# Kernel tuning notes

Hardware: AMD Instinct MI355X
Metric: run time of the kernel (lower is better)

Reference implementation:

```python
import jax, jax.numpy as jnp
import numpy as np

EPS = 1e-5

def mish(x):
    return x * jnp.tanh(jnp.logaddexp(x, 0.0))

def instance_norm(x, gamma, beta):
    # x: (N, C, D, H, W); normalize per (N, C) over spatial dims
    mu = jnp.mean(x, axis=(2, 3, 4), keepdims=True)
    var = jnp.var(x, axis=(2, 3, 4), keepdims=True)
    xh = (x - mu) * jax.lax.rsqrt(var + EPS)
    return xh * gamma[None, :, None, None, None] + beta[None, :, None, None, None]

def conv3d(x, w, stride, padding):
    return jax.lax.conv_general_dilated(
        x, w, window_strides=(stride, stride, stride), padding=padding,
        dimension_numbers=('NCDHW', 'OIDHW', 'NCDHW'))

def pad_k(k, p):
    # center-pad kernel spatial dims up to 5x5x5
    return jnp.pad(k, ((0, 0), (0, 0), (p, p), (p, p), (p, p)))

def mode_conv(x, t, c5, c3, c1, a3, a5, gw, gb, gamma, beta):
    N = x.shape[0]
    Co = c5.shape[0]
    # gate: Linear(num_tasks -> 5*Co), softmax over the 5 experts
    g = jax.nn.softmax((t @ gw.T + gb).reshape(N, 5, Co), axis=1)  # (N,5,Co)
    pool3 = jnp.full((3, 3, 3), 1.0 / 27.0, x.dtype)
    pool5 = jnp.full((5, 5, 5), 1.0 / 125.0, x.dtype)
    experts = jnp.stack([
        c5,                      # conv5x5
        pad_k(c3, 1),            # conv3x3 padded to 5
        pad_k(c1, 2),            # conv1x1 padded to 5
        pad_k(a3 * pool3, 1),    # avg3x3: (Co,Ci,1,1,1)*(3,3,3) broadcast, padded
        a5 * pool5,              # avg5x5
    ], axis=0)                   # (5, Co, Ci, 5, 5, 5)
    # per-sample synthesized kernel
    w = jnp.einsum('eoidhw,neo->noidhw', experts, g)  # (N, Co, Ci, 5,5,5)
    # per-sample conv3d, padding 'same' (training branch of original)
    y = jax.vmap(lambda xi, wi: conv3d(xi[None], wi, 1, 'SAME')[0])(x, w)
    return mish(instance_norm(y, gamma, beta))

def setup_inputs() -> dict:
    key = jax.random.key(0)
    ks = jax.random.split(key, 32)
    N, Ci, Co, T = 2, 32, 64, 10
    D = H = W = 64
    f32 = jnp.float32
    def kconv(k, co, ci, ksz, fan):
        bound = float(np.sqrt(6.0 / ((1.0 + 5.0) * fan)))  # kaiming_uniform a=sqrt(5), fan_out
        return jax.random.uniform(k, (co, ci, ksz, ksz, ksz), f32, -bound, bound)
    inp = {}
    inp['x'] = jax.random.normal(ks[0], (N, Ci, D, H, W), f32)
    inp['t'] = jax.random.normal(ks[1], (N, T), f32)
    def layer(base, ci, co):
        p = {}
        p['conv5'] = kconv(ks[base + 0], co, ci, 5, co * 125)
        p['conv3'] = kconv(ks[base + 1], co, ci, 3, co * 27)
        p['conv1'] = kconv(ks[base + 2], co, ci, 1, co)
        p['avg3'] = kconv(ks[base + 3], co, ci, 1, co)
        p['avg5'] = kconv(ks[base + 4], co, ci, 1, co)
        gb_bound = 1.0 / np.sqrt(T)
        p['gw'] = jax.random.uniform(ks[base + 5], (5 * co, T), f32, -gb_bound, gb_bound)
        p['gb'] = jax.random.uniform(ks[base + 6], (5 * co,), f32, -gb_bound, gb_bound)
        p['gamma'] = jnp.ones((co,), f32)
        p['beta'] = jnp.zeros((co,), f32)
        return p
    for name, v in layer(2, Ci, Co).items():
        inp['l1_' + name] = v
    for name, v in layer(12, Co, Co).items():
        inp['l2_' + name] = v
    dw_bound = float(np.sqrt(1.0 / (Co * 8)))
    inp['down_w'] = jax.random.uniform(ks[25], (Co, Co, 2, 2, 2), f32, -dw_bound, dw_bound)
    inp['down_gamma'] = jnp.ones((Co,), f32)
    inp['down_beta'] = jnp.zeros((Co,), f32)
    return inp

def reference(x, t,
              l1_conv5, l1_conv3, l1_conv1, l1_avg3, l1_avg5, l1_gw, l1_gb, l1_gamma, l1_beta,
              l2_conv5, l2_conv3, l2_conv1, l2_avg3, l2_avg5, l2_gw, l2_gb, l2_gamma, l2_beta,
              down_w, down_gamma, down_beta):
    h = mode_conv(x, t, l1_conv5, l1_conv3, l1_conv1, l1_avg3, l1_avg5, l1_gw, l1_gb, l1_gamma, l1_beta)
    x_skip = mode_conv(h, t, l2_conv5, l2_conv3, l2_conv1, l2_avg3, l2_avg5, l2_gw, l2_gb, l2_gamma, l2_beta)
    y = conv3d(x_skip, down_w, 2, 'VALID')
    y = mish(instance_norm(y, down_gamma, down_beta))
    return (y, x_skip)
```

## Files before the change

kernel.cpp:

```cpp
#include <hip/hip_runtime.h>
#include <cstdint>
#include <cstddef>

constexpr int NB  = 2;
constexpr int CO  = 64;
constexpr int DIM = 64;
constexpr int SP  = DIM * DIM * DIM;
constexpr int NC  = NB * CO;
constexpr int Y_SZ = NB * CO * 32 * 32 * 32;

typedef float f32x4 __attribute__((ext_vector_type(4)));
typedef short s16x8 __attribute__((ext_vector_type(8)));

__device__ __forceinline__ unsigned short f2bf(float f) {
    unsigned int u = __float_as_uint(f);
    unsigned int r = (u + 0x7fffu + ((u >> 16) & 1u)) >> 16;
    return (unsigned short)r;
}
__device__ __forceinline__ float bf2f(unsigned short u) {
    return __uint_as_float((unsigned int)u << 16);
}
__device__ __forceinline__ unsigned int pack2(float a, float b) {
    return (unsigned int)f2bf(a) | ((unsigned int)f2bf(b) << 16);
}
__device__ __forceinline__ float mish_f(float x) {
    float e = __expf(x);
    float num = e * (e + 2.f);
    float r = x * num * __builtin_amdgcn_rcpf(num + 2.f);
    return (x > 15.f) ? x : r;
}

__device__ __forceinline__ void gload_lds16(const void* g, void* l) {
    __builtin_amdgcn_global_load_lds(
        (const __attribute__((address_space(1))) unsigned int*)g,
        (__attribute__((address_space(3))) unsigned int*)l, 16, 0, 0);
}

__global__ void gate_kernel(const float* __restrict__ t, const float* __restrict__ gw,
                            const float* __restrict__ gb, float* __restrict__ g,
                            float* __restrict__ zbuf) {
    int tid = threadIdx.x;
    if (tid >= 128) { if (tid < 192) zbuf[tid - 128] = 0.f; return; }
    int n = tid >> 6, co = tid & 63;
    float tl[10];
#pragma unroll
    for (int k = 0; k < 10; ++k) tl[k] = t[n * 10 + k];
    float l[5];
#pragma unroll
    for (int e = 0; e < 5; ++e) {
        int row = e * CO + co;
        float acc = gb[row];
#pragma unroll
        for (int k = 0; k < 10; ++k) acc += tl[k] * gw[row * 10 + k];
        l[e] = acc;
    }
    float m = l[0];
#pragma unroll
    for (int e = 1; e < 5; ++e) m = fmaxf(m, l[e]);
    float s = 0.f;
#pragma unroll
    for (int e = 0; e < 5; ++e) { l[e] = expf(l[e] - m); s += l[e]; }
    float inv = 1.f / s;
#pragma unroll
    for (int e = 0; e < 5; ++e) g[(n * 5 + e) * CO + co] = l[e] * inv;
}

template <int CI>
__global__ void synth_kernel(const float* __restrict__ g,
                             const float* __restrict__ c5, const float* __restrict__ c3,
                             const float* __restrict__ c1, const float* __restrict__ a3,
                             const float* __restrict__ a5, unsigned short* __restrict__ wbuf) {
    int idx = blockIdx.x * 256 + threadIdx.x;
    constexpr int TOTAL = NB * CO * CI * 125;
    if (idx >= TOTAL) return;
    int tap = idx % 125;
    int ci  = (idx / 125) % CI;
    int co  = (idx / (125 * CI)) % CO;
    int n   = idx / (125 * CI * CO);
    const float* gn = g + n * 5 * CO;
    float g0 = gn[0 * CO + co], g1 = gn[1 * CO + co], g2 = gn[2 * CO + co],
          g3 = gn[3 * CO + co], g4 = gn[4 * CO + co];
    int dz = tap / 25, dy = (tap / 5) % 5, dx = tap % 5;
    int oc = co * CI + ci;
    float v = g0 * c5[(size_t)oc * 125 + tap] + g4 * a5[oc] * (1.f / 125.f);
    if (dz >= 1 && dz <= 3 && dy >= 1 && dy <= 3 && dx >= 1 && dx <= 3)
        v += g1 * c3[(size_t)oc * 27 + (dz - 1) * 9 + (dy - 1) * 3 + (dx - 1)]
           + g3 * a3[oc] * (1.f / 27.f);
    if (dz == 2 && dy == 2 && dx == 2) v += g2 * c1[oc];
    int t = (dy * 5 + dx);
    int cich = ci >> 5, cil = ci & 31;
    wbuf[((((size_t)(n * 5 + dz) * (CI / 32) + cich) * 25 + t) * 64 + co) * 32 + cil] = f2bf(v);
}

__global__ __launch_bounds__(256) void x_to_cl(const float* __restrict__ x,
                                               unsigned short* __restrict__ xcl) {
    __shared__ float ld[32][256];
    int b = blockIdx.x;
    int n = b >> 10;
    size_t base = (size_t)(b & 1023) * 256;
    int tid = threadIdx.x;
    const float* xp = x + (size_t)n * 32 * SP + base + tid;
#pragma unroll
    for (int c = 0; c < 32; ++c) ld[c][tid] = xp[(size_t)c * SP];
    __syncthreads();
    uint4* op = (uint4*)(xcl + ((size_t)n * SP + base) * 32);
#pragma unroll
    for (int r = 0; r < 4; ++r) {
        int idx = r * 256 + tid;
        int px = idx >> 2, q = idx & 3;
        uint4 o;
        o.x = pack2(ld[q * 8 + 0][px], ld[q * 8 + 1][px]);
        o.y = pack2(ld[q * 8 + 2][px], ld[q * 8 + 3][px]);
        o.z = pack2(ld[q * 8 + 4][px], ld[q * 8 + 5][px]);
        o.w = pack2(ld[q * 8 + 6][px], ld[q * 8 + 7][px]);
        op[idx] = o;
    }
}

template <int CI, bool OUT_CL, int PCH>
__global__ __launch_bounds__(512, 4) void conv5_mfma(const unsigned short* __restrict__ xin,
                                                     const unsigned short* __restrict__ wbuf,
                                                     void* __restrict__ outp,
                                                     float* __restrict__ part,
                                                     const void* __restrict__ zbuf) {
    constexpr int NCH = CI / 32;
    constexpr int NS  = 5 * NCH;
    __shared__ __align__(16) unsigned short lds[2][12800];

    const int b   = blockIdx.x;
    const int xt  = b & 3;
    const int yt  = (b >> 2) & 3;
    const int z   = (b >> 4) & 63;
    const int n   = b >> 10;
    const int tid = threadIdx.x;
    const int lane = tid & 63, wv = tid >> 6;
    const int xl = lane & 15, kh = lane >> 4;
    const int yh = wv >> 2, cq = wv & 3;

    f32x4 acc[8];
#pragma unroll
    for (int pt = 0; pt < 8; ++pt)
#pragma unroll
        for (int j = 0; j < 4; ++j) acc[pt][j] = 0.f;

    long goff[4]; int gval[4];
#pragma unroll
    for (int r = 0; r < 4; ++r) {
        int idx = tid + r * 512;
        int p = idx >> 2, khs = idx & 3;
        int xx = p % 20, yy = p / 20;
        int yi = yt * 16 - 2 + yy, xi = xt * 16 - 2 + xx;
        gval[r] = ((unsigned)yi < 64u) && ((unsigned)xi < 64u);
        goff[r] = ((long)(yi * 64 + xi) * CI + khs * 8) * 2;
    }

    auto stage = [&](int s, int buf) {
        int dz = s / NCH, cich = s % NCH;
        int zi = z + dz - 2;
        bool zok = (unsigned)zi < 64u;
        const char* pb = (const char*)xin
                       + ((size_t)(n * SP + zi * 4096) * CI + cich * 32) * 2;
        char* lb = (char*)&lds[buf][0];
#pragma unroll
        for (int r = 0; r < 4; ++r) {
            int idx = tid + r * 512;
            if (idx < 1600) {
                const void* g = (zok && gval[r]) ? (const void*)(pb + goff[r]) : zbuf;
                gload_lds16(g, lb + idx * 16);
            }
        }
    };

    auto compute = [&](int s, int buf) {
        int dz = s / NCH, cich = s % NCH;
        const unsigned short* wp = wbuf
            + ((size_t)((n * 5 + dz) * NCH + cich) * 25) * 2048
            + cq * 512 + xl * 32 + kh * 8;
        const char* src = (const char*)&lds[buf][0];
        __builtin_amdgcn_s_setprio(1);
#pragma unroll 1
        for (int dx = 0; dx < 5; ++dx) {
            int xx = xl + dx;
            s16x8 fr[12];
#pragma unroll
            for (int r = 0; r < 12; ++r) {
                int row = yh * 8 + r;
                fr[r] = *(const s16x8*)(src + (size_t)(row * 20 + xx) * 64 + kh * 16);
            }
#pragma unroll
            for (int dy = 0; dy < 5; ++dy) {
                s16x8 a = *(const s16x8*)(wp + (size_t)(dy * 5 + dx) * 2048);
#pragma unroll
                for (int pt = 0; pt < 8; ++pt)
                    acc[pt] = __builtin_amdgcn_mfma_f32_16x16x32_bf16(
                        a, fr[pt + dy], acc[pt], 0, 0, 0);
            }
        }
        __builtin_amdgcn_s_setprio(0);
    };

    stage(0, 0);
    __syncthreads();
#pragma unroll 1
    for (int s = 0; s < NS; ++s) {
        if (s + 1 < NS) stage(s + 1, (s + 1) & 1);
        compute(s, s & 1);
        __syncthreads();
    }

    {
        float s1[4], s2[4];
#pragma unroll
        for (int j = 0; j < 4; ++j) { s1[j] = 0.f; s2[j] = 0.f; }
#pragma unroll
        for (int pt = 0; pt < 8; ++pt)
#pragma unroll
            for (int j = 0; j < 4; ++j) {
                float v = acc[pt][j];
                s1[j] += v; s2[j] += v * v;
            }
#pragma unroll
        for (int o = 1; o < 16; o <<= 1)
#pragma unroll
            for (int j = 0; j < 4; ++j) {
                s1[j] += __shfl_xor(s1[j], o, 64);
                s2[j] += __shfl_xor(s2[j], o, 64);
            }
        if (xl == 0) {
            int co = cq * 16 + kh * 4;
            int cb = (b & 1023) * 2 + yh;
#pragma unroll
            for (int j = 0; j < 4; ++j) {
                part[((size_t)(n * 2 + 0) * 64 + co + j) * PCH + cb] = s1[j];
                part[((size_t)(n * 2 + 1) * 64 + co + j) * PCH + cb] = s2[j];
            }
        }
    }

    if (OUT_CL) {
        char* tb = (char*)&lds[0][0];
#pragma unroll
        for (int pt = 0; pt < 8; ++pt) {
            int pix = (yh * 8 + pt) * 16 + xl;
            unsigned int ad = ((unsigned)(pix * 128 + cq * 32 + kh * 8))
                              ^ ((unsigned)(pix & 7) << 4);
            *(unsigned int*)(tb + ad)     = pack2(acc[pt][0], acc[pt][1]);
            *(unsigned int*)(tb + ad + 4) = pack2(acc[pt][2], acc[pt][3]);
        }
        __syncthreads();
#pragma unroll
        for (int it = 0; it < 4; ++it) {
            int idx = it * 512 + tid;
            int pix = idx >> 3, ch = idx & 7;
            uint4 v = *(const uint4*)(tb + (((unsigned)idx * 16)
                                            ^ ((unsigned)(pix & 7) << 4)));
            int y = yt * 16 + (pix >> 4), x = xt * 16 + (pix & 15);
            *(uint4*)((unsigned short*)outp
                      + ((size_t)(n * SP + z * 4096 + y * 64 + x) * 64 + ch * 8)) = v;
        }
    } else {
        float* op = (float*)outp;
#pragma unroll
        for (int pt = 0; pt < 8; ++pt) {
            int y = yt * 16 + yh * 8 + pt;
#pragma unroll
            for (int j = 0; j < 4; ++j)
                op[((size_t)(n * 64 + cq * 16 + kh * 4 + j) * 64 + z) * 4096
                   + y * 64 + xt * 16 + xl] = acc[pt][j];
        }
    }
}

template <int CH>
__global__ void stats_fin(const float* __restrict__ part, float* __restrict__ st,
                          float invS) {
    int blk = blockIdx.x;
    int n = blk >> 6, co = blk & 63;
    int tid = threadIdx.x;
    const float* ps = part + ((size_t)(n * 2 + 0) * 64 + co) * CH;
    const float* pq = part + ((size_t)(n * 2 + 1) * 64 + co) * CH;
    float s1 = 0.f, s2 = 0.f;
    for (int i = tid; i < CH; i += 256) { s1 += ps[i]; s2 += pq[i]; }
#pragma unroll
    for (int o = 1; o < 64; o <<= 1) {
        s1 += __shfl_xor(s1, o, 64);
        s2 += __shfl_xor(s2, o, 64);
    }
    __shared__ float sh1[4], sh2[4];
    if ((tid & 63) == 0) { sh1[tid >> 6] = s1; sh2[tid >> 6] = s2; }
    __syncthreads();
    if (tid == 0) {
        float a = sh1[0] + sh1[1] + sh1[2] + sh1[3];
        float q = sh2[0] + sh2[1] + sh2[2] + sh2[3];
        float mean = a * invS;
        float var  = q * invS - mean * mean;
        st[(n * 64 + co) * 2]     = mean;
        st[(n * 64 + co) * 2 + 1] = rsqrtf(var + 1e-5f);
    }
}

__global__ void norm_mish_cl_kernel(unsigned short* __restrict__ h,
                                    const float* __restrict__ st,
                                    const float* __restrict__ gamma,
                                    const float* __restrict__ beta) {
    size_t idx = (size_t)blockIdx.x * 256 + threadIdx.x;
    uint4 v = ((uint4*)h)[idx];
    int c0 = ((int)(idx & 7)) * 8;
    size_t pix = idx >> 3;
    int n = (int)(pix >> 18);
    unsigned int* pv = &v.x;
#pragma unroll
    for (int q = 0; q < 4; ++q) {
        unsigned int wv = pv[q];
        unsigned int out = 0;
#pragma unroll
        for (int hv = 0; hv < 2; ++hv) {
            int c = c0 + 2 * q + hv;
            int nc = n * 64 + c;
            float val = bf2f((unsigned short)((wv >> (16 * hv)) & 0xffffu));
            float xh = (val - st[nc * 2]) * st[nc * 2 + 1] * gamma[c] + beta[c];
            out |= ((unsigned int)f2bf(mish_f(xh))) << (16 * hv);
        }
        pv[q] = out;
    }
    ((uint4*)h)[idx] = v;
}

template <int SHIFT>
__global__ void norm_mish_kernel(float* __restrict__ buf, const float* __restrict__ stats,
                                 const float* __restrict__ gamma, const float* __restrict__ beta,
                                 int total4) {
    int idx = blockIdx.x * 256 + threadIdx.x;
    if (idx >= total4) return;
    float4 v = reinterpret_cast<float4*>(buf)[idx];
    int nc = idx >> (SHIFT - 2);
    int c  = nc & 63;
    float mean = stats[nc * 2], inv = stats[nc * 2 + 1];
    float ga = gamma[c], be = beta[c];
    float* pv = &v.x;
#pragma unroll
    for (int k = 0; k < 4; ++k) {
        float xh = (pv[k] - mean) * inv * ga + be;
        pv[k] = mish_f(xh);
    }
    reinterpret_cast<float4*>(buf)[idx] = v;
}

__global__ __launch_bounds__(256) void down_conv_kernel(float* __restrict__ xin,
                                                        const float* __restrict__ dw,
                                                        const float* __restrict__ st,
                                                        const float* __restrict__ gamma,
                                                        const float* __restrict__ beta,
                                                        float* __restrict__ out,
                                                        float* __restrict__ part) {
    __shared__ float ls[8][2][8][64];
    int b   = blockIdx.x;
    int yt  = b & 7;
    int z   = (b >> 3) & 31;
    int n   = b >> 8;
    int tid = threadIdx.x;
    int xo  = tid & 31;
    int cog = tid >> 5;

    float acc[4][8];
#pragma unroll
    for (int yo = 0; yo < 4; ++yo)
#pragma unroll
        for (int j = 0; j < 8; ++j) acc[yo][j] = 0.f;

    for (int cc = 0; cc < 8; ++cc) {
        for (int idx = tid; idx < 8192; idx += 256) {
            int xx = idx & 63;
            int yy = (idx >> 6) & 7;
            int dz = (idx >> 9) & 1;
            int c  = idx >> 10;
            int ci = cc * 8 + c;
            size_t ga = ((size_t)(n * CO + ci) * 64 + 2 * z + dz) * 4096
                      + (yt * 8 + yy) * 64 + xx;
            float v = xin[ga];
            int nc = n * 64 + ci;
            float nv = mish_f((v - st[nc * 2]) * st[nc * 2 + 1] * gamma[ci] + beta[ci]);
            ls[c][dz][yy][xx] = nv;
            xin[ga] = nv;
        }
        __syncthreads();
#pragma unroll 1
        for (int c = 0; c < 8; ++c) {
            int ci = cc * 8 + c;
#pragma unroll
            for (int tap = 0; tap < 8; ++tap) {
                int dz = tap >> 2, dy = (tap >> 1) & 1, dx = tap & 1;
                float w[8];
#pragma unroll
                for (int j = 0; j < 8; ++j)
                    w[j] = dw[((size_t)(cog * 8 + j) * CO + ci) * 8 + tap];
#pragma unroll
                for (int yo = 0; yo < 4; ++yo) {
                    float xv = ls[c][dz][yo * 2 + dy][2 * xo + dx];
#pragma unroll
                    for (int j = 0; j < 8; ++j) acc[yo][j] += w[j] * xv;
                }
            }
        }
        __syncthreads();
    }
#pragma unroll
    for (int yo = 0; yo < 4; ++yo)
#pragma unroll
        for (int j = 0; j < 8; ++j)
            out[((size_t)(n * CO + cog * 8 + j) * 32 + z) * 1024 + (yt * 4 + yo) * 32 + xo]
                = acc[yo][j];

    float s1[8], s2[8];
#pragma unroll
    for (int j = 0; j < 8; ++j) { s1[j] = 0.f; s2[j] = 0.f; }
#pragma unroll
    for (int yo = 0; yo < 4; ++yo)
#pragma unroll
        for (int j = 0; j < 8; ++j) {
            float v = acc[yo][j];
            s1[j] += v; s2[j] += v * v;
        }
#pragma unroll
    for (int o = 1; o < 32; o <<= 1)
#pragma unroll
        for (int j = 0; j < 8; ++j) {
            s1[j] += __shfl_xor(s1[j], o, 64);
            s2[j] += __shfl_xor(s2[j], o, 64);
        }
    if (xo == 0) {
        int cb = b & 255;
#pragma unroll
        for (int j = 0; j < 8; ++j) {
            int co = cog * 8 + j;
            part[((size_t)(n * 2 + 0) * 64 + co) * 256 + cb] = s1[j];
            part[((size_t)(n * 2 + 1) * 64 + co) * 256 + cb] = s2[j];
        }
    }
}

extern "C" void kernel_launch(void* const* d_in, const int* in_sizes, int n_in,
                              void* d_out, int out_size, void* d_ws, size_t ws_size,
                              hipStream_t stream) {
    const float* x      = (const float*)d_in[0];
    const float* t      = (const float*)d_in[1];
    const float* l1_c5  = (const float*)d_in[2];
    const float* l1_c3  = (const float*)d_in[3];
    const float* l1_c1  = (const float*)d_in[4];
    const float* l1_a3  = (const float*)d_in[5];
    const float* l1_a5  = (const float*)d_in[6];
    const float* l1_gw  = (const float*)d_in[7];
    const float* l1_gb  = (const float*)d_in[8];
    const float* l1_ga  = (const float*)d_in[9];
    const float* l1_be  = (const float*)d_in[10];
    const float* l2_c5  = (const float*)d_in[11];
    const float* l2_c3  = (const float*)d_in[12];
    const float* l2_c1  = (const float*)d_in[13];
    const float* l2_a3  = (const float*)d_in[14];
    const float* l2_a5  = (const float*)d_in[15];
    const float* l2_gw  = (const float*)d_in[16];
    const float* l2_gb  = (const float*)d_in[17];
    const float* l2_ga  = (const float*)d_in[18];
    const float* l2_be  = (const float*)d_in[19];
    const float* down_w = (const float*)d_in[20];
    const float* dn_ga  = (const float*)d_in[21];
    const float* dn_be  = (const float*)d_in[22];

    char* ws = (char*)d_ws;
    unsigned short* xcl = (unsigned short*)(ws);
    unsigned short* h2  = (unsigned short*)(ws + 33554432);
    unsigned short* w1  = (unsigned short*)(ws + 100663296);
    unsigned short* w2  = (unsigned short*)(ws + 101687296);
    float* g1    = (float*)(ws + 103735296);
    float* g2    = (float*)(ws + 103737856);
    float* st1   = (float*)(ws + 103740416);
    float* st2   = (float*)(ws + 103741440);
    float* st3   = (float*)(ws + 103742464);
    float* part1 = (float*)(ws + 103743488);
    float* part2 = (float*)(ws + 105840640);
    float* part3 = (float*)(ws + 107937792);
    float* zbuf  = (float*)(ws + 108199936);

    float* yout  = (float*)d_out;
    float* xskip = (float*)d_out + Y_SZ;

    gate_kernel<<<1, 192, 0, stream>>>(t, l1_gw, l1_gb, g1, zbuf);
    gate_kernel<<<1, 192, 0, stream>>>(t, l2_gw, l2_gb, g2, zbuf);
    synth_kernel<32><<<(NB * CO * 32 * 125 + 255) / 256, 256, 0, stream>>>(
        g1, l1_c5, l1_c3, l1_c1, l1_a3, l1_a5, w1);
    synth_kernel<64><<<(NB * CO * 64 * 125 + 255) / 256, 256, 0, stream>>>(
        g2, l2_c5, l2_c3, l2_c1, l2_a3, l2_a5, w2);
    x_to_cl<<<2048, 256, 0, stream>>>(x, xcl);

    conv5_mfma<32, true, 2048><<<2048, 512, 0, stream>>>(xcl, w1, h2, part1, zbuf);
    stats_fin<2048><<<128, 256, 0, stream>>>(part1, st1, 1.f / SP);
    norm_mish_cl_kernel<<<16384, 256, 0, stream>>>(h2, st1, l1_ga, l1_be);

    conv5_mfma<64, false, 2048><<<2048, 512, 0, stream>>>(h2, w2, xskip, part2, zbuf);
    stats_fin<2048><<<128, 256, 0, stream>>>(part2, st2, 1.f / SP);

    down_conv_kernel<<<NB * 32 * 8, 256, 0, stream>>>(xskip, down_w, st2, l2_ga, l2_be,
                                                      yout, part3);
    stats_fin<256><<<128, 256, 0, stream>>>(part3, st3, 1.f / 32768.f);
    norm_mish_kernel<15><<<(NC * 32768 / 4 + 255) / 256, 256, 0, stream>>>(
        yout, st3, dn_ga, dn_be, NC * 32768 / 4);
}
```

Before: 851.5 us.

## Store second conv output as bf16 channels-last and fuse launch stages

The second conv now writes its output as a bf16 channels-last buffer instead of fp32 NCDHW. The down-conv kernel reads that buffer with vector loads, applies norm+mish, and writes the fp32 x_skip. The gate and synth kernels are merged into single launches, and the conv block index is remapped by a stride-8 swizzle. This cuts conv2 write traffic and the down-conv read-modify-write, but the down-conv's scattered fp32 stores to x_skip may be poorly coalesced. Rounding the conv2 output to bf16 before normalization also adds precision loss.

```diff
diff --git a/kernel.cpp b/kernel.cpp
--- a/kernel.cpp
+++ b/kernel.cpp
@@ -36,12 +36,20 @@
         (__attribute__((address_space(3))) unsigned int*)l, 16, 0, 0);
 }
 
-__global__ void gate_kernel(const float* __restrict__ t, const float* __restrict__ gw,
-                            const float* __restrict__ gb, float* __restrict__ g,
-                            float* __restrict__ zbuf) {
+__global__ void gate2_kernel(const float* __restrict__ t,
+                             const float* __restrict__ gw1, const float* __restrict__ gb1,
+                             float* __restrict__ g1,
+                             const float* __restrict__ gw2, const float* __restrict__ gb2,
+                             float* __restrict__ g2,
+                             float* __restrict__ zbuf) {
     int tid = threadIdx.x;
-    if (tid >= 128) { if (tid < 192) zbuf[tid - 128] = 0.f; return; }
-    int n = tid >> 6, co = tid & 63;
+    if (tid < 64) zbuf[tid] = 0.f;
+    int layer = tid >> 7;
+    int lt = tid & 127;
+    int n = lt >> 6, co = lt & 63;
+    const float* gw = layer ? gw2 : gw1;
+    const float* gb = layer ? gb2 : gb1;
+    float* g = layer ? g2 : g1;
     float tl[10];
 #pragma unroll
     for (int k = 0; k < 10; ++k) tl[k] = t[n * 10 + k];
@@ -66,13 +74,11 @@
 }
 
 template <int CI>
-__global__ void synth_kernel(const float* __restrict__ g,
-                             const float* __restrict__ c5, const float* __restrict__ c3,
-                             const float* __restrict__ c1, const float* __restrict__ a3,
-                             const float* __restrict__ a5, unsigned short* __restrict__ wbuf) {
-    int idx = blockIdx.x * 256 + threadIdx.x;
-    constexpr int TOTAL = NB * CO * CI * 125;
-    if (idx >= TOTAL) return;
+__device__ __forceinline__ void synth_one(int idx, const float* __restrict__ g,
+                                          const float* __restrict__ c5, const float* __restrict__ c3,
+                                          const float* __restrict__ c1, const float* __restrict__ a3,
+                                          const float* __restrict__ a5,
+                                          unsigned short* __restrict__ wbuf) {
     int tap = idx % 125;
     int ci  = (idx / 125) % CI;
     int co  = (idx / (125 * CI)) % CO;
@@ -92,6 +98,23 @@
     wbuf[((((size_t)(n * 5 + dz) * (CI / 32) + cich) * 25 + t) * 64 + co) * 32 + cil] = f2bf(v);
 }
 
+__global__ void synth2_kernel(const float* __restrict__ g1,
+                              const float* __restrict__ c51, const float* __restrict__ c31,
+                              const float* __restrict__ c11, const float* __restrict__ a31,
+                              const float* __restrict__ a51, unsigned short* __restrict__ w1,
+                              const float* __restrict__ g2,
+                              const float* __restrict__ c52, const float* __restrict__ c32,
+                              const float* __restrict__ c12, const float* __restrict__ a32,
+                              const float* __restrict__ a52, unsigned short* __restrict__ w2) {
+    constexpr int T1 = NB * CO * 32 * 125;
+    constexpr int T2 = NB * CO * 64 * 125;
+    int idx = blockIdx.x * 256 + threadIdx.x;
+    if (idx < T1)
+        synth_one<32>(idx, g1, c51, c31, c11, a31, a51, w1);
+    else if (idx < T1 + T2)
+        synth_one<64>(idx - T1, g2, c52, c32, c12, a32, a52, w2);
+}
+
 __global__ __launch_bounds__(256) void x_to_cl(const float* __restrict__ x,
                                                unsigned short* __restrict__ xcl) {
     __shared__ float ld[32][256];
@@ -117,17 +140,18 @@
     }
 }
 
-template <int CI, bool OUT_CL, int PCH>
+template <int CI, int PCH>
 __global__ __launch_bounds__(512, 4) void conv5_mfma(const unsigned short* __restrict__ xin,
                                                      const unsigned short* __restrict__ wbuf,
-                                                     void* __restrict__ outp,
+                                                     unsigned short* __restrict__ outp,
                                                      float* __restrict__ part,
                                                      const void* __restrict__ zbuf) {
     constexpr int NCH = CI / 32;
     constexpr int NS  = 5 * NCH;
     __shared__ __align__(16) unsigned short lds[2][12800];
 
-    const int b   = blockIdx.x;
+    const int bid = blockIdx.x;
+    const int b   = (bid & 7) * 256 + (bid >> 3);
     const int xt  = b & 3;
     const int yt  = (b >> 2) & 3;
     const int z   = (b >> 4) & 63;
@@ -237,7 +261,7 @@
         }
     }
 
-    if (OUT_CL) {
+    {
         char* tb = (char*)&lds[0][0];
 #pragma unroll
         for (int pt = 0; pt < 8; ++pt) {
@@ -255,18 +279,8 @@
             uint4 v = *(const uint4*)(tb + (((unsigned)idx * 16)
                                             ^ ((unsigned)(pix & 7) << 4)));
             int y = yt * 16 + (pix >> 4), x = xt * 16 + (pix & 15);
-            *(uint4*)((unsigned short*)outp
+            *(uint4*)(outp
                       + ((size_t)(n * SP + z * 4096 + y * 64 + x) * 64 + ch * 8)) = v;
-        }
-    } else {
-        float* op = (float*)outp;
-#pragma unroll
-        for (int pt = 0; pt < 8; ++pt) {
-            int y = yt * 16 + yh * 8 + pt;
-#pragma unroll
-            for (int j = 0; j < 4; ++j)
-                op[((size_t)(n * 64 + cq * 16 + kh * 4 + j) * 64 + z) * 4096
-                   + y * 64 + xt * 16 + xl] = acc[pt][j];
         }
     }
 }
@@ -346,11 +360,12 @@
     reinterpret_cast<float4*>(buf)[idx] = v;
 }
 
-__global__ __launch_bounds__(256) void down_conv_kernel(float* __restrict__ xin,
+__global__ __launch_bounds__(256) void down_conv_kernel(const unsigned short* __restrict__ h3,
                                                         const float* __restrict__ dw,
                                                         const float* __restrict__ st,
                                                         const float* __restrict__ gamma,
                                                         const float* __restrict__ beta,
+                                                        float* __restrict__ xskip,
                                                         float* __restrict__ out,
                                                         float* __restrict__ part) {
     __shared__ float ls[8][2][8][64];
@@ -369,19 +384,28 @@
         for (int j = 0; j < 8; ++j) acc[yo][j] = 0.f;
 
     for (int cc = 0; cc < 8; ++cc) {
-        for (int idx = tid; idx < 8192; idx += 256) {
-            int xx = idx & 63;
-            int yy = (idx >> 6) & 7;
-            int dz = (idx >> 9) & 1;
-            int c  = idx >> 10;
-            int ci = cc * 8 + c;
-            size_t ga = ((size_t)(n * CO + ci) * 64 + 2 * z + dz) * 4096
-                      + (yt * 8 + yy) * 64 + xx;
-            float v = xin[ga];
-            int nc = n * 64 + ci;
-            float nv = mish_f((v - st[nc * 2]) * st[nc * 2 + 1] * gamma[ci] + beta[ci]);
-            ls[c][dz][yy][xx] = nv;
-            xin[ga] = nv;
+#pragma unroll
+        for (int r = 0; r < 4; ++r) {
+            int p  = r * 256 + tid;
+            int xx = p & 63, yy = (p >> 6) & 7, dz = p >> 9;
+            int zi = 2 * z + dz, yi = yt * 8 + yy;
+            size_t pix = (size_t)n * SP + (size_t)zi * 4096 + yi * 64 + xx;
+            uint4 v = *(const uint4*)(h3 + pix * 64 + cc * 8);
+            unsigned int* pv = &v.x;
+#pragma unroll
+            for (int q = 0; q < 4; ++q) {
+#pragma unroll
+                for (int hv = 0; hv < 2; ++hv) {
+                    int c  = 2 * q + hv;
+                    int ci = cc * 8 + c;
+                    int nc = n * 64 + ci;
+                    float val = bf2f((unsigned short)((pv[q] >> (16 * hv)) & 0xffffu));
+                    float nv  = mish_f((val - st[nc * 2]) * st[nc * 2 + 1] * gamma[ci]
+                                       + beta[ci]);
+                    ls[c][dz][yy][xx] = nv;
+                    xskip[((size_t)(n * CO + ci) * 64 + zi) * 4096 + yi * 64 + xx] = nv;
+                }
+            }
         }
         __syncthreads();
 #pragma unroll 1
@@ -468,39 +492,37 @@
 
     char* ws = (char*)d_ws;
     unsigned short* xcl = (unsigned short*)(ws);
-    unsigned short* h2  = (unsigned short*)(ws + 33554432);
-    unsigned short* w1  = (unsigned short*)(ws + 100663296);
-    unsigned short* w2  = (unsigned short*)(ws + 101687296);
-    float* g1    = (float*)(ws + 103735296);
-    float* g2    = (float*)(ws + 103737856);
-    float* st1   = (float*)(ws + 103740416);
-    float* st2   = (float*)(ws + 103741440);
-    float* st3   = (float*)(ws + 103742464);
-    float* part1 = (float*)(ws + 103743488);
-    float* part2 = (float*)(ws + 105840640);
-    float* part3 = (float*)(ws + 107937792);
-    float* zbuf  = (float*)(ws + 108199936);
+    unsigned short* h3  = (unsigned short*)(ws);
+    float* part1 = (float*)(ws + 33554432);
+    unsigned short* h2  = (unsigned short*)(ws + 67108864);
+    unsigned short* w1  = (unsigned short*)(ws + 134217728);
+    unsigned short* w2  = (unsigned short*)(ws + 135241728);
+    float* part2 = (float*)(ws + 137289728);
+    float* part3 = (float*)(ws + 139386880);
+    float* g1    = (float*)(ws + 139649024);
+    float* g2    = (float*)(ws + 139651584);
+    float* st1   = (float*)(ws + 139654144);
+    float* st2   = (float*)(ws + 139655168);
+    float* st3   = (float*)(ws + 139656192);
+    float* zbuf  = (float*)(ws + 139657216);
 
     float* yout  = (float*)d_out;
     float* xskip = (float*)d_out + Y_SZ;
 
-    gate_kernel<<<1, 192, 0, stream>>>(t, l1_gw, l1_gb, g1, zbuf);
-    gate_kernel<<<1, 192, 0, stream>>>(t, l2_gw, l2_gb, g2, zbuf);
-    synth_kernel<32><<<(NB * CO * 32 * 125 + 255) / 256, 256, 0, stream>>>(
-        g1, l1_c5, l1_c3, l1_c1, l1_a3, l1_a5, w1);
-    synth_kernel<64><<<(NB * CO * 64 * 125 + 255) / 256, 256, 0, stream>>>(
-        g2, l2_c5, l2_c3, l2_c1, l2_a3, l2_a5, w2);
+    gate2_kernel<<<1, 256, 0, stream>>>(t, l1_gw, l1_gb, g1, l2_gw, l2_gb, g2, zbuf);
+    synth2_kernel<<<6000, 256, 0, stream>>>(g1, l1_c5, l1_c3, l1_c1, l1_a3, l1_a5, w1,
+                                            g2, l2_c5, l2_c3, l2_c1, l2_a3, l2_a5, w2);
     x_to_cl<<<2048, 256, 0, stream>>>(x, xcl);
 
-    conv5_mfma<32, true, 2048><<<2048, 512, 0, stream>>>(xcl, w1, h2, part1, zbuf);
+    conv5_mfma<32, 2048><<<2048, 512, 0, stream>>>(xcl, w1, h2, part1, zbuf);
     stats_fin<2048><<<128, 256, 0, stream>>>(part1, st1, 1.f / SP);
     norm_mish_cl_kernel<<<16384, 256, 0, stream>>>(h2, st1, l1_ga, l1_be);
 
-    conv5_mfma<64, false, 2048><<<2048, 512, 0, stream>>>(h2, w2, xskip, part2, zbuf);
+    conv5_mfma<64, 2048><<<2048, 512, 0, stream>>>(h2, w2, h3, part2, zbuf);
     stats_fin<2048><<<128, 256, 0, stream>>>(part2, st2, 1.f / SP);
 
-    down_conv_kernel<<<NB * 32 * 8, 256, 0, stream>>>(xskip, down_w, st2, l2_ga, l2_be,
-                                                      yout, part3);
+    down_conv_kernel<<<NB * 32 * 8, 256, 0, stream>>>(h3, down_w, st2, l2_ga, l2_be,
+                                                      xskip, yout, part3);
     stats_fin<256><<<128, 256, 0, stream>>>(part3, st3, 1.f / 32768.f);
     norm_mish_kernel<15><<<(NC * 32768 / 4 + 255) / 256, 256, 0, stream>>>(
         yout, st3, dn_ga, dn_be, NC * 32768 / 4);
```

Result: faster. 798.8 us (-6.2%).
